# Performance work log

Measured on AMD Instinct MI355X. Metric: run time of the kernel, lower is better.

The kernel has to match this reference:

```python
import jax, jax.numpy as jnp
import numpy as np

ITERATIONS = 10
LAMBDA0 = 0.01


def skew(v):
    # (..., 3) -> (..., 3, 3) skew-symmetric matrices
    x, y, z = v[..., 0], v[..., 1], v[..., 2]
    o = jnp.zeros_like(x)
    return jnp.stack([
        jnp.stack([o, -z, y], -1),
        jnp.stack([z, o, -x], -1),
        jnp.stack([-y, x, o], -1)], -2)


def so3exp_map(w):
    # Rodrigues formula, numerically safe near theta=0
    theta2 = jnp.sum(w * w) + 1e-12
    theta = jnp.sqrt(theta2)
    W = skew(w)
    A = jnp.sin(theta) / theta
    B = (1.0 - jnp.cos(theta)) / theta2
    return jnp.eye(3, dtype=w.dtype) + A * W + B * (W @ W)


def sobel_filter(img):
    # img: (C, H, W) -> (gx, gy) each (C, H, W); depthwise conv, zero pad
    C = img.shape[0]
    kx = jnp.array([[-1., 0., 1.], [-2., 0., 2.], [-1., 0., 1.]], img.dtype)
    k = jnp.stack([kx, kx.T], 0)                       # (2,3,3)
    kern = jnp.broadcast_to(k[None, :, None], (C, 2, 1, 3, 3)).reshape(2 * C, 1, 3, 3)
    out = jax.lax.conv_general_dilated(img[None], kern, (1, 1), 'SAME',
                                       feature_group_count=C)[0]
    return out[0::2], out[1::2]


def from_homogeneous(x):
    return x[..., :-1] / x[..., -1:]


def _forward(q_matrix, r_matrix, points_2d, points_3d, query_feat, reference_feat, K1, size_ratio):
    C, H, W = query_feat.shape
    rel = q_matrix @ jnp.linalg.inv(r_matrix)
    R = rel[:3, :3]
    t = rel[3, :3]  # faithful to original (bottom row)
    gx, gy = sobel_filter(query_feat)

    idx0 = jnp.floor(points_2d / size_ratio).astype(jnp.int32)
    ix0 = jnp.clip(idx0[:, 0], 0, W - 1)
    iy0 = jnp.clip(idx0[:, 1], 0, H - 1)
    feat0 = reference_feat[:, iy0, ix0].T              # (N, C)

    pts_h = jnp.concatenate([points_3d, jnp.ones_like(points_3d[:, :1])], -1)
    pts0 = from_homogeneous(pts_h @ r_matrix.T)        # (N, 3)

    fx, fy = K1[0, 0], K1[1, 1]
    N = pts0.shape[0]
    I3 = jnp.broadcast_to(jnp.eye(3, dtype=pts0.dtype), (N, 3, 3))

    def gather_idx(p2d):
        ii = jnp.floor(p2d / size_ratio).astype(jnp.int32)
        return jnp.clip(ii[:, 0], 0, W - 1), jnp.clip(ii[:, 1], 0, H - 1)

    def step(carry, i):
        R, t, lam, prev = carry
        pts1 = pts0 @ R + t                            # (N, 3) (faithful: R, not R.T)
        ix, iy = gather_idx(from_homogeneous(pts1 @ K1.T))
        err = query_feat[:, iy, ix].T - feat0          # (N, C)
        cost = jnp.sum(err * err, -1)                  # squared_loss, weights = 1
        prev = jnp.where(i == 0, cost.mean(), prev)

        J_p_T = jnp.concatenate([I3, -skew(pts1)], -1)  # (N, 3, 6)
        x, y, z = pts1[:, 0], pts1[:, 1], pts1[:, 2]
        o, zz = jnp.ones_like(x), jnp.zeros_like(x)
        J_h_p = jnp.stack([o * fx, zz, -fx * x / z,
                           zz, o * fy, -fy * y / z], -1).reshape(N, 2, 3)
        J_h_p = J_h_p / z[:, None, None] / size_ratio   # (N, 2, 3)
        gxf = gx[:, iy, ix].T
        gyf = gy[:, iy, ix].T
        J_e_h = jnp.stack([gxf, gyf], -1)               # (N, C, 2)
        J = jnp.einsum('ncu,nuk->nck', J_e_h, J_h_p @ J_p_T)  # (N, C, 6)

        g = jnp.einsum('nck,nc->k', J, err)             # (6,)
        Hs = jnp.einsum('nck,ncl->kl', J, J)            # (6, 6)
        D = jnp.diag(jnp.diag(Hs) + 1e-9)
        delta = -(jnp.linalg.inv(Hs + D * lam) @ g)

        dt, dw = delta[:3], delta[3:6]
        dr = so3exp_map(dw)
        R_new = dr @ R
        t_new = dr @ t + dt
        npts = pts0 @ R_new.T + t_new
        jx, jy = gather_idx(from_homogeneous(npts @ K1.T))
        nerr = query_feat[:, jy, jx].T - feat0
        ncost = jnp.sum(nerr * nerr, -1).mean()

        bad = jnp.isnan(ncost) | jnp.any(jnp.isnan(delta))
        worse = ncost > prev
        lam_upd = jnp.clip(lam * jnp.where(worse, 10., 0.1), 1e-6, 100.)
        lam = jnp.where(bad, lam, lam_upd)
        accept = jnp.logical_not(worse | bad)
        R = jnp.where(accept, R_new, R)
        t = jnp.where(accept, t_new, t)
        prev = jnp.where(accept, ncost, prev)
        return (R, t, lam, prev), None

    lam0 = jnp.asarray(LAMBDA0, pts0.dtype)
    prev0 = jnp.asarray(jnp.inf, pts0.dtype)
    (R, t, _, _), _ = jax.lax.scan(step, (R, t, lam0, prev0), jnp.arange(ITERATIONS))
    return R, t


def setup_inputs() -> dict:
    key = jax.random.key(0)
    k1, k2, k3, k4, k5 = jax.random.split(key, 5)
    N, C, H, W = 8192, 1024, 128, 128
    size_ratio = 8
    f, cx, cy = 1200.0, 512.0, 512.0
    K1 = jnp.array([[f, 0., cx], [0., f, cy], [0., 0., 1.]], jnp.float32)
    # 3D points whose identity-pose projection lands inside the 1024px image
    uv = jax.random.uniform(k1, (N, 2), jnp.float32, 100.0, 900.0)
    z = jax.random.uniform(k2, (N, 1), jnp.float32, 4.0, 8.0)
    points_3d = jnp.concatenate([(uv - jnp.array([cx, cy])) / f * z, z], -1)
    points_2d = jax.random.uniform(k3, (N, 2), jnp.float32, 0.0, 1023.0)
    query_feat = jax.random.normal(k4, (C, H, W), jnp.float32) * 0.1
    reference_feat = jax.random.normal(k5, (C, H, W), jnp.float32) * 0.1
    return {
        'q_matrix': jnp.eye(4, dtype=jnp.float32),
        'r_matrix': jnp.eye(4, dtype=jnp.float32),
        'points_2d': points_2d,
        'points_3d': points_3d,
        'query_feat': query_feat,
        'reference_feat': reference_feat,
        'K1': K1,
        'size_ratio': size_ratio,
    }


def reference(q_matrix, r_matrix, points_2d, points_3d, query_feat, reference_feat, K1, size_ratio):
    return _forward(q_matrix, r_matrix, points_2d, points_3d, query_feat,
                    reference_feat, K1, size_ratio)
```

## Files before the change

kernel.cpp:

```cpp
#include <hip/hip_runtime.h>
#include <math.h>

constexpr int C_  = 1024;
constexpr int H_  = 128;
constexpr int W_  = 128;
constexpr int HW_ = H_ * W_;
constexpr int N_  = 8192;
constexpr int NCOMP = 28;
constexpr int ITERS = 10;


__global__ void k_init(const float* __restrict__ q, const float* __restrict__ r,
                       const float* __restrict__ K1, const int* __restrict__ srp,
                       float* __restrict__ st) {
    if (threadIdx.x != 0 || blockIdx.x != 0) return;
    double a[4][8];
    for (int i = 0; i < 4; i++)
        for (int j = 0; j < 4; j++) { a[i][j] = r[i*4+j]; a[i][j+4] = (i == j) ? 1.0 : 0.0; }
    for (int col = 0; col < 4; col++) {
        int piv = col; double mx = fabs(a[col][col]);
        for (int i = col+1; i < 4; i++) if (fabs(a[i][col]) > mx) { mx = fabs(a[i][col]); piv = i; }
        if (piv != col) for (int j = 0; j < 8; j++) { double t = a[col][j]; a[col][j] = a[piv][j]; a[piv][j] = t; }
        double d = a[col][col];
        for (int j = 0; j < 8; j++) a[col][j] /= d;
        for (int i = 0; i < 4; i++) if (i != col) {
            double f = a[i][col];
            for (int j = 0; j < 8; j++) a[i][j] -= f * a[col][j];
        }
    }
    double rel[4][4];
    for (int i = 0; i < 4; i++)
        for (int j = 0; j < 4; j++) {
            double s = 0;
            for (int k = 0; k < 4; k++) s += (double)q[i*4+k] * a[k][j+4];
            rel[i][j] = s;
        }
    for (int i = 0; i < 3; i++)
        for (int j = 0; j < 3; j++) st[i*3+j] = (float)rel[i][j];
    st[9]  = (float)rel[3][0];
    st[10] = (float)rel[3][1];
    st[11] = (float)rel[3][2];
    st[12] = 0.01f;
    st[13] = __builtin_inff();
    for (int i = 0; i < 9; i++) st[32+i] = K1[i];
    st[41] = K1[0]; st[42] = K1[4];
    st[43] = (float)srp[0];
}

__global__ void k_pts0(const float* __restrict__ p3d, const float* __restrict__ p2d,
                       const float* __restrict__ r, const int* __restrict__ srp,
                       float* __restrict__ pts0, int* __restrict__ pix0) {
    int n = blockIdx.x * blockDim.x + threadIdx.x;
    if (n >= N_) return;
    float sr = (float)srp[0];
    float ph[4] = { p3d[n*3+0], p3d[n*3+1], p3d[n*3+2], 1.f };
    float h[4];
    for (int i = 0; i < 4; i++) {
        float s = 0.f;
        for (int j = 0; j < 4; j++) s += r[i*4+j] * ph[j];
        h[i] = s;
    }
    pts0[n*3+0] = h[0]/h[3];
    pts0[n*3+1] = h[1]/h[3];
    pts0[n*3+2] = h[2]/h[3];
    int ix = (int)floorf(p2d[n*2+0] / sr); ix = min(max(ix, 0), W_-1);
    int iy = (int)floorf(p2d[n*2+1] / sr); iy = min(max(iy, 0), H_-1);
    pix0[n] = iy * W_ + ix;
}

template <bool SOBEL>
__global__ void k_transpose2(const float* __restrict__ src, float* __restrict__ dq,
                             float* __restrict__ dgx, float* __restrict__ dgy) {
    constexpr int CT = 16, YT = 8, XT = 32;
    constexpr int RS = YT + 2;
    constexpr int CS = XT + 2;
    constexpr int PCS = 35;
    constexpr int CHS = RS * PCS + 1;
    __shared__ float lds[CT * CHS];
    const int x0 = blockIdx.x * XT;
    const int y0 = blockIdx.y * YT;
    const int cc = blockIdx.z * CT;
    const int tid = threadIdx.x;
    for (int idx = tid; idx < CT * RS * CS; idx += 256) {
        int c   = idx / (RS * CS);
        int rem = idx % (RS * CS);
        int r   = rem / CS;
        int x   = rem % CS;
        int gy  = y0 + r - 1;
        int gx  = x0 + x - 1;
        float v = 0.f;
        if (gy >= 0 && gy < H_ && gx >= 0 && gx < W_)
            v = src[(size_t)(cc + c) * HW_ + gy * W_ + gx];
        lds[c * CHS + r * PCS + x] = v;
    }
    __syncthreads();
    const int c       = tid & 15;
    const int s       = tid >> 4;
    const int row     = s >> 1;
    const int colbase = (s & 1) * 16;
    const float* Lt = &lds[c * CHS + row * PCS + colbase];
    const float* Lm = Lt + PCS;
    const float* Lb = Lm + PCS;
    size_t o = ((size_t)((y0 + row) * W_ + x0 + colbase)) * C_ + cc + c;
    if (!SOBEL) {
        for (int cx = 0; cx < 16; cx++, o += C_)
            dq[o] = Lm[cx + 1];
    } else {
        float t0l = Lt[0], t0m = Lt[1];
        float t1l = Lm[0], t1m = Lm[1];
        float t2l = Lb[0], t2m = Lb[1];
        for (int cx = 0; cx < 16; cx++, o += C_) {
            float t0r = Lt[cx + 2];
            float t1r = Lm[cx + 2];
            float t2r = Lb[cx + 2];
            dq[o]  = t1m;
            dgx[o] = (t0r - t0l) + 2.f*(t1r - t1l) + (t2r - t2l);
            dgy[o] = (t2l + 2.f*t2m + t2r) - (t0l + 2.f*t0m + t0r);
            t0l = t0m; t0m = t0r;
            t1l = t1m; t1m = t1r;
            t2l = t2m; t2m = t2r;
        }
    }
}

__global__ void k_feat0(const float* __restrict__ rT, const int* __restrict__ pix0,
                        float* __restrict__ feat0) {
    int n = blockIdx.x;
    const float4* s = (const float4*)(rT + (size_t)pix0[n] * C_);
    float4* d = (float4*)(feat0 + (size_t)n * C_);
    d[threadIdx.x] = s[threadIdx.x];
}

__device__ inline float waveSum(float v) {
    for (int o = 32; o; o >>= 1) v += __shfl_down(v, o, 64);
    return v;
}

__global__ void k_passA(const float* __restrict__ qT, const float* __restrict__ gxT,
                        const float* __restrict__ gyT, const float* __restrict__ feat0,
                        const float* __restrict__ pts0, const float* __restrict__ st,
                        float* __restrict__ parts) {
    const int n = blockIdx.x;
    const int tid = threadIdx.x;
    const float p0 = pts0[n*3+0], p1 = pts0[n*3+1], p2 = pts0[n*3+2];
    const float X = p0*st[0] + p1*st[3] + p2*st[6] + st[9];
    const float Y = p0*st[1] + p1*st[4] + p2*st[7] + st[10];
    const float Z = p0*st[2] + p1*st[5] + p2*st[8] + st[11];
    const float hx = st[32]*X + st[33]*Y + st[34]*Z;
    const float hy = st[35]*X + st[36]*Y + st[37]*Z;
    const float hz = st[38]*X + st[39]*Y + st[40]*Z;
    const float sr = st[43];
    const float u = hx / hz, v = hy / hz;
    int ix = (int)floorf(u / sr); ix = min(max(ix, 0), W_-1);
    int iy = (int)floorf(v / sr); iy = min(max(iy, 0), H_-1);
    const int pix = iy * W_ + ix;

    const float4* q4 = (const float4*)(qT  + (size_t)pix * C_);
    const float4* g4 = (const float4*)(gxT + (size_t)pix * C_);
    const float4* h4 = (const float4*)(gyT + (size_t)pix * C_);
    const float4* f4 = (const float4*)(feat0 + (size_t)n * C_);
    float4 qv = q4[tid], gv = g4[tid], yv = h4[tid], fv = f4[tid];

    float cost = 0, bx = 0, by = 0, mxx = 0, mxy = 0, myy = 0;
    {
        float e;
        e = qv.x - fv.x; cost += e*e; bx += gv.x*e; by += yv.x*e; mxx += gv.x*gv.x; mxy += gv.x*yv.x; myy += yv.x*yv.x;
        e = qv.y - fv.y; cost += e*e; bx += gv.y*e; by += yv.y*e; mxx += gv.y*gv.y; mxy += gv.y*yv.y; myy += yv.y*yv.y;
        e = qv.z - fv.z; cost += e*e; bx += gv.z*e; by += yv.z*e; mxx += gv.z*gv.z; mxy += gv.z*yv.z; myy += yv.z*yv.z;
        e = qv.w - fv.w; cost += e*e; bx += gv.w*e; by += yv.w*e; mxx += gv.w*gv.w; mxy += gv.w*yv.w; myy += yv.w*yv.w;
    }
    cost = waveSum(cost); bx = waveSum(bx); by = waveSum(by);
    mxx = waveSum(mxx); mxy = waveSum(mxy); myy = waveSum(myy);

    __shared__ float red[4][6];
    int wid = tid >> 6, lane = tid & 63;
    if (lane == 0) {
        red[wid][0] = cost; red[wid][1] = bx;  red[wid][2] = by;
        red[wid][3] = mxx;  red[wid][4] = mxy; red[wid][5] = myy;
    }
    __syncthreads();
    if (tid == 0) {
        cost = red[0][0]+red[1][0]+red[2][0]+red[3][0];
        bx   = red[0][1]+red[1][1]+red[2][1]+red[3][1];
        by   = red[0][2]+red[1][2]+red[2][2]+red[3][2];
        mxx  = red[0][3]+red[1][3]+red[2][3]+red[3][3];
        mxy  = red[0][4]+red[1][4]+red[2][4]+red[3][4];
        myy  = red[0][5]+red[1][5]+red[2][5]+red[3][5];

        const float fx = st[41], fy = st[42];
        const float s = 1.f / (Z * sr);
        const float jh00 = fx, jh02 = -fx * X / Z;
        const float jh11 = fy, jh12 = -fy * Y / Z;
        float A0[6], A1[6];
        A0[0] = s*jh00; A0[1] = 0.f;    A0[2] = s*jh02;
        A0[3] = s*(jh02*Y); A0[4] = s*(jh00*Z - jh02*X); A0[5] = s*(-jh00*Y);
        A1[0] = 0.f;    A1[1] = s*jh11; A1[2] = s*jh12;
        A1[3] = s*(-jh11*Z + jh12*Y); A1[4] = s*(-jh12*X); A1[5] = s*(jh11*X);

        parts[0*N_ + n] = cost;
        for (int k = 0; k < 6; k++) parts[(1+k)*N_ + n] = A0[k]*bx + A1[k]*by;
        int idx = 7;
        for (int k = 0; k < 6; k++)
            for (int l = k; l < 6; l++) {
                parts[idx*N_ + n] = A0[k]*A0[l]*mxx + (A0[k]*A1[l] + A1[k]*A0[l])*mxy + A1[k]*A1[l]*myy;
                idx++;
            }
    }
}

__global__ void k_reduce_solve(const float* __restrict__ parts, float* __restrict__ st,
                               int iter) {
    const int tid = threadIdx.x;
    const int w = tid >> 6, lane = tid & 63;
    for (int comp = w; comp < NCOMP; comp += 16) {
        const float4* p4 = (const float4*)(parts + (size_t)comp * N_);
        double s = 0;
        for (int i = lane; i < N_/4; i += 64) {
            float4 v = p4[i];
            s += (double)v.x + (double)v.y + (double)v.z + (double)v.w;
        }
        for (int o = 32; o; o >>= 1) s += __shfl_down(s, o, 64);
        if (lane == 0) st[44 + comp] = (float)s;
    }
    __syncthreads();
    if (tid != 0) return;

    double costsum = st[44];
    if (iter == 0) st[13] = (float)(costsum / (double)N_);
    double g[6];
    for (int k = 0; k < 6; k++) g[k] = st[45+k];
    double Hs[6][6];
    int idx = 51;
    for (int k = 0; k < 6; k++)
        for (int l = k; l < 6; l++) { Hs[k][l] = st[idx]; Hs[l][k] = st[idx]; idx++; }
    double lam = st[12];
    double M[6][7];
    for (int i = 0; i < 6; i++) {
        for (int j = 0; j < 6; j++) M[i][j] = Hs[i][j];
        M[i][i] += (Hs[i][i] + 1e-9) * lam;
        M[i][6] = -g[i];
    }
    for (int col = 0; col < 6; col++) {
        int piv = col; double mx = fabs(M[col][col]);
        for (int i = col+1; i < 6; i++) if (fabs(M[i][col]) > mx) { mx = fabs(M[i][col]); piv = i; }
        if (piv != col) for (int j = col; j < 7; j++) { double t = M[col][j]; M[col][j] = M[piv][j]; M[piv][j] = t; }
        double d = M[col][col];
        for (int j = col; j < 7; j++) M[col][j] /= d;
        for (int i = 0; i < 6; i++) if (i != col) {
            double f = M[i][col];
            if (f != 0.0) for (int j = col; j < 7; j++) M[i][j] -= f * M[col][j];
        }
    }
    double delta[6];
    int bad = 0;
    for (int i = 0; i < 6; i++) {
        delta[i] = M[i][6];
        st[26+i] = (float)delta[i];
        if (isnan(st[26+i])) bad = 1;
    }
    st[72] = (float)bad;
    double w0 = delta[3], w1 = delta[4], w2 = delta[5];
    double th2 = w0*w0 + w1*w1 + w2*w2 + 1e-12;
    double th = sqrt(th2);
    double Af = sin(th) / th, Bf = (1.0 - cos(th)) / th2;
    double Wm[3][3] = {{0,-w2,w1},{w2,0,-w0},{-w1,w0,0}};
    double W2[3][3];
    for (int i = 0; i < 3; i++)
        for (int j = 0; j < 3; j++) {
            double s2 = 0;
            for (int k = 0; k < 3; k++) s2 += Wm[i][k]*Wm[k][j];
            W2[i][j] = s2;
        }
    double dr[3][3];
    for (int i = 0; i < 3; i++)
        for (int j = 0; j < 3; j++)
            dr[i][j] = (i == j ? 1.0 : 0.0) + Af*Wm[i][j] + Bf*W2[i][j];
    double Rn[3][3];
    for (int i = 0; i < 3; i++)
        for (int j = 0; j < 3; j++) {
            double s2 = 0;
            for (int k = 0; k < 3; k++) s2 += dr[i][k] * (double)st[k*3+j];
            Rn[i][j] = s2;
        }
    for (int i = 0; i < 3; i++)
        for (int j = 0; j < 3; j++) st[14 + i*3 + j] = (float)Rn[i][j];
    for (int i = 0; i < 3; i++) {
        double s2 = 0;
        for (int k = 0; k < 3; k++) s2 += dr[i][k] * (double)st[9+k];
        st[23+i] = (float)(s2 + delta[i]);
    }
}

__global__ void k_passB(const float* __restrict__ qT, const float* __restrict__ feat0,
                        const float* __restrict__ pts0, const float* __restrict__ st,
                        float* __restrict__ ncost) {
    const int n = blockIdx.x;
    const int tid = threadIdx.x;
    const float p0 = pts0[n*3+0], p1 = pts0[n*3+1], p2 = pts0[n*3+2];
    const float X = p0*st[14] + p1*st[15] + p2*st[16] + st[23];
    const float Y = p0*st[17] + p1*st[18] + p2*st[19] + st[24];
    const float Z = p0*st[20] + p1*st[21] + p2*st[22] + st[25];
    const float hx = st[32]*X + st[33]*Y + st[34]*Z;
    const float hy = st[35]*X + st[36]*Y + st[37]*Z;
    const float hz = st[38]*X + st[39]*Y + st[40]*Z;
    const float sr = st[43];
    const float u = hx / hz, v = hy / hz;
    int ix = (int)floorf(u / sr); ix = min(max(ix, 0), W_-1);
    int iy = (int)floorf(v / sr); iy = min(max(iy, 0), H_-1);
    const int pix = iy * W_ + ix;

    const float4* q4 = (const float4*)(qT + (size_t)pix * C_);
    const float4* f4 = (const float4*)(feat0 + (size_t)n * C_);
    float4 qv = q4[tid], fv = f4[tid];
    float cost = 0, e;
    e = qv.x - fv.x; cost += e*e;
    e = qv.y - fv.y; cost += e*e;
    e = qv.z - fv.z; cost += e*e;
    e = qv.w - fv.w; cost += e*e;
    cost = waveSum(cost);
    __shared__ float red[4];
    int wid = tid >> 6, lane = tid & 63;
    if (lane == 0) red[wid] = cost;
    __syncthreads();
    if (tid == 0) ncost[n] = red[0] + red[1] + red[2] + red[3];
}

__global__ void k_decide(const float* __restrict__ ncost, float* __restrict__ st) {
    const int tid = threadIdx.x;
    double s = 0;
    for (int i = tid; i < N_; i += 256) s += (double)ncost[i];
    __shared__ double sd[256];
    sd[tid] = s;
    __syncthreads();
    for (int k = 128; k; k >>= 1) { if (tid < k) sd[tid] += sd[tid+k]; __syncthreads(); }
    if (tid == 0) {
        float nc = (float)(sd[0] / (double)N_);
        float prev = st[13], lam = st[12];
        bool bad = isnan(nc) || (st[72] != 0.f);
        bool worse = nc > prev;
        float lu = lam * (worse ? 10.f : 0.1f);
        lu = fminf(fmaxf(lu, 1e-6f), 100.f);
        st[12] = bad ? lam : lu;
        bool accept = !(worse || bad);
        if (accept) {
            for (int i = 0; i < 9; i++) st[i] = st[14+i];
            for (int i = 0; i < 3; i++) st[9+i] = st[23+i];
            st[13] = nc;
        }
    }
}

__global__ void k_out(const float* __restrict__ st, float* __restrict__ out) {
    int i = threadIdx.x;
    if (i < 12) out[i] = st[i];
}

extern "C" void kernel_launch(void* const* d_in, const int* in_sizes, int n_in,
                              void* d_out, int out_size, void* d_ws, size_t ws_size,
                              hipStream_t stream) {
    const float* q   = (const float*)d_in[0];
    const float* r   = (const float*)d_in[1];
    const float* p2d = (const float*)d_in[2];
    const float* p3d = (const float*)d_in[3];
    const float* qf  = (const float*)d_in[4];
    const float* rf  = (const float*)d_in[5];
    const float* K1  = (const float*)d_in[6];
    const int*   srp = (const int*)d_in[7];

    float* ws = (float*)d_ws;
    size_t off = 0;
    float* qT    = ws + off; off += (size_t)HW_ * C_;
    float* gxT   = ws + off; off += (size_t)HW_ * C_;
    float* gyT   = ws + off; off += (size_t)HW_ * C_;
    float* feat0 = ws + off; off += (size_t)N_ * C_;
    float* pts0  = ws + off; off += 3 * N_;
    int*   pix0  = (int*)(ws + off); off += N_;
    float* parts = ws + off; off += (size_t)NCOMP * N_;
    float* ncost = ws + off; off += N_;
    float* st    = ws + off; off += 128;

    k_init<<<1, 1, 0, stream>>>(q, r, K1, srp, st);
    k_pts0<<<(N_ + 255) / 256, 256, 0, stream>>>(p3d, p2d, r, srp, pts0, pix0);
    k_transpose2<false><<<dim3(W_/32, H_/8, C_/16), 256, 0, stream>>>(rf, qT, nullptr, nullptr);
    k_feat0<<<N_, 256, 0, stream>>>(qT, pix0, feat0);
    k_transpose2<true><<<dim3(W_/32, H_/8, C_/16), 256, 0, stream>>>(qf, qT, gxT, gyT);

    for (int it = 0; it < ITERS; it++) {
        k_passA<<<N_, 256, 0, stream>>>(qT, gxT, gyT, feat0, pts0, st, parts);
        k_reduce_solve<<<1, 1024, 0, stream>>>(parts, st, it);
        k_passB<<<N_, 256, 0, stream>>>(qT, feat0, pts0, st, ncost);
        k_decide<<<1, 256, 0, stream>>>(ncost, st);
    }
    k_out<<<1, 64, 0, stream>>>(st, (float*)d_out);
}
```

Measured before the change: 1.049 ms.

## Map one wavefront per point, pre-reduce per block, merge setup kernels

Each 256-thread block now handles four points, one wavefront each, instead of one point per block. Wave reductions use xor shuffles, and the 28 Jacobian/Hessian components are computed in parallel across lanes and summed per block. This shrinks the partial-sum buffers that the single-block solve and decide kernels read by a factor of four. k_init and k_pts0 are merged into one launch, and the transpose tile height is halved to double the number of blocks. The cost is extra per-block shared-memory syncs, and the floating-point summation order changes.

```diff
diff --git a/kernel.cpp b/kernel.cpp
--- a/kernel.cpp
+++ b/kernel.cpp
@@ -8,70 +8,70 @@
 constexpr int N_  = 8192;
 constexpr int NCOMP = 28;
 constexpr int ITERS = 10;
-
-
-__global__ void k_init(const float* __restrict__ q, const float* __restrict__ r,
-                       const float* __restrict__ K1, const int* __restrict__ srp,
-                       float* __restrict__ st) {
-    if (threadIdx.x != 0 || blockIdx.x != 0) return;
-    double a[4][8];
-    for (int i = 0; i < 4; i++)
-        for (int j = 0; j < 4; j++) { a[i][j] = r[i*4+j]; a[i][j+4] = (i == j) ? 1.0 : 0.0; }
-    for (int col = 0; col < 4; col++) {
-        int piv = col; double mx = fabs(a[col][col]);
-        for (int i = col+1; i < 4; i++) if (fabs(a[i][col]) > mx) { mx = fabs(a[i][col]); piv = i; }
-        if (piv != col) for (int j = 0; j < 8; j++) { double t = a[col][j]; a[col][j] = a[piv][j]; a[piv][j] = t; }
-        double d = a[col][col];
-        for (int j = 0; j < 8; j++) a[col][j] /= d;
-        for (int i = 0; i < 4; i++) if (i != col) {
-            double f = a[i][col];
-            for (int j = 0; j < 8; j++) a[i][j] -= f * a[col][j];
-        }
-    }
-    double rel[4][4];
-    for (int i = 0; i < 4; i++)
-        for (int j = 0; j < 4; j++) {
-            double s = 0;
-            for (int k = 0; k < 4; k++) s += (double)q[i*4+k] * a[k][j+4];
-            rel[i][j] = s;
-        }
-    for (int i = 0; i < 3; i++)
-        for (int j = 0; j < 3; j++) st[i*3+j] = (float)rel[i][j];
-    st[9]  = (float)rel[3][0];
-    st[10] = (float)rel[3][1];
-    st[11] = (float)rel[3][2];
-    st[12] = 0.01f;
-    st[13] = __builtin_inff();
-    for (int i = 0; i < 9; i++) st[32+i] = K1[i];
-    st[41] = K1[0]; st[42] = K1[4];
-    st[43] = (float)srp[0];
-}
-
-__global__ void k_pts0(const float* __restrict__ p3d, const float* __restrict__ p2d,
-                       const float* __restrict__ r, const int* __restrict__ srp,
-                       float* __restrict__ pts0, int* __restrict__ pix0) {
+constexpr int NB_ = 2048;
+
+
+__global__ void k_setup(const float* __restrict__ q, const float* __restrict__ r,
+                        const float* __restrict__ K1, const int* __restrict__ srp,
+                        const float* __restrict__ p3d, const float* __restrict__ p2d,
+                        float* __restrict__ st, float* __restrict__ pts0,
+                        int* __restrict__ pix0) {
     int n = blockIdx.x * blockDim.x + threadIdx.x;
-    if (n >= N_) return;
-    float sr = (float)srp[0];
-    float ph[4] = { p3d[n*3+0], p3d[n*3+1], p3d[n*3+2], 1.f };
-    float h[4];
-    for (int i = 0; i < 4; i++) {
-        float s = 0.f;
-        for (int j = 0; j < 4; j++) s += r[i*4+j] * ph[j];
-        h[i] = s;
-    }
-    pts0[n*3+0] = h[0]/h[3];
-    pts0[n*3+1] = h[1]/h[3];
-    pts0[n*3+2] = h[2]/h[3];
-    int ix = (int)floorf(p2d[n*2+0] / sr); ix = min(max(ix, 0), W_-1);
-    int iy = (int)floorf(p2d[n*2+1] / sr); iy = min(max(iy, 0), H_-1);
-    pix0[n] = iy * W_ + ix;
+    if (n < N_) {
+        float sr = (float)srp[0];
+        float ph[4] = { p3d[n*3+0], p3d[n*3+1], p3d[n*3+2], 1.f };
+        float h[4];
+        for (int i = 0; i < 4; i++) {
+            float s = 0.f;
+            for (int j = 0; j < 4; j++) s += r[i*4+j] * ph[j];
+            h[i] = s;
+        }
+        pts0[n*3+0] = h[0]/h[3];
+        pts0[n*3+1] = h[1]/h[3];
+        pts0[n*3+2] = h[2]/h[3];
+        int ix = (int)floorf(p2d[n*2+0] / sr); ix = min(max(ix, 0), W_-1);
+        int iy = (int)floorf(p2d[n*2+1] / sr); iy = min(max(iy, 0), H_-1);
+        pix0[n] = iy * W_ + ix;
+    }
+    if (blockIdx.x == 0 && threadIdx.x == 0) {
+        double a[4][8];
+        for (int i = 0; i < 4; i++)
+            for (int j = 0; j < 4; j++) { a[i][j] = r[i*4+j]; a[i][j+4] = (i == j) ? 1.0 : 0.0; }
+        for (int col = 0; col < 4; col++) {
+            int piv = col; double mx = fabs(a[col][col]);
+            for (int i = col+1; i < 4; i++) if (fabs(a[i][col]) > mx) { mx = fabs(a[i][col]); piv = i; }
+            if (piv != col) for (int j = 0; j < 8; j++) { double t = a[col][j]; a[col][j] = a[piv][j]; a[piv][j] = t; }
+            double d = a[col][col];
+            for (int j = 0; j < 8; j++) a[col][j] /= d;
+            for (int i = 0; i < 4; i++) if (i != col) {
+                double f = a[i][col];
+                for (int j = 0; j < 8; j++) a[i][j] -= f * a[col][j];
+            }
+        }
+        double rel[4][4];
+        for (int i = 0; i < 4; i++)
+            for (int j = 0; j < 4; j++) {
+                double s = 0;
+                for (int k = 0; k < 4; k++) s += (double)q[i*4+k] * a[k][j+4];
+                rel[i][j] = s;
+            }
+        for (int i = 0; i < 3; i++)
+            for (int j = 0; j < 3; j++) st[i*3+j] = (float)rel[i][j];
+        st[9]  = (float)rel[3][0];
+        st[10] = (float)rel[3][1];
+        st[11] = (float)rel[3][2];
+        st[12] = 0.01f;
+        st[13] = __builtin_inff();
+        for (int i = 0; i < 9; i++) st[32+i] = K1[i];
+        st[41] = K1[0]; st[42] = K1[4];
+        st[43] = (float)srp[0];
+    }
 }
 
 template <bool SOBEL>
 __global__ void k_transpose2(const float* __restrict__ src, float* __restrict__ dq,
                              float* __restrict__ dgx, float* __restrict__ dgy) {
-    constexpr int CT = 16, YT = 8, XT = 32;
+    constexpr int CT = 16, YT = 4, XT = 32;
     constexpr int RS = YT + 2;
     constexpr int CS = XT + 2;
     constexpr int PCS = 35;
@@ -96,20 +96,20 @@
     __syncthreads();
     const int c       = tid & 15;
     const int s       = tid >> 4;
-    const int row     = s >> 1;
-    const int colbase = (s & 1) * 16;
+    const int row     = s >> 2;
+    const int colbase = (s & 3) * 8;
     const float* Lt = &lds[c * CHS + row * PCS + colbase];
     const float* Lm = Lt + PCS;
     const float* Lb = Lm + PCS;
     size_t o = ((size_t)((y0 + row) * W_ + x0 + colbase)) * C_ + cc + c;
     if (!SOBEL) {
-        for (int cx = 0; cx < 16; cx++, o += C_)
+        for (int cx = 0; cx < 8; cx++, o += C_)
             dq[o] = Lm[cx + 1];
     } else {
         float t0l = Lt[0], t0m = Lt[1];
         float t1l = Lm[0], t1m = Lm[1];
         float t2l = Lb[0], t2m = Lb[1];
-        for (int cx = 0; cx < 16; cx++, o += C_) {
+        for (int cx = 0; cx < 8; cx++, o += C_) {
             float t0r = Lt[cx + 2];
             float t1r = Lm[cx + 2];
             float t2r = Lb[cx + 2];
@@ -123,25 +123,28 @@
     }
 }
 
-__global__ void k_feat0(const float* __restrict__ rT, const int* __restrict__ pix0,
-                        float* __restrict__ feat0) {
-    int n = blockIdx.x;
+__global__ __launch_bounds__(256) void k_feat0(const float* __restrict__ rT,
+                                               const int* __restrict__ pix0,
+                                               float* __restrict__ feat0) {
+    const int w = threadIdx.x >> 6, lane = threadIdx.x & 63;
+    const int n = blockIdx.x * 4 + w;
     const float4* s = (const float4*)(rT + (size_t)pix0[n] * C_);
     float4* d = (float4*)(feat0 + (size_t)n * C_);
-    d[threadIdx.x] = s[threadIdx.x];
-}
-
-__device__ inline float waveSum(float v) {
-    for (int o = 32; o; o >>= 1) v += __shfl_down(v, o, 64);
-    return v;
-}
-
-__global__ void k_passA(const float* __restrict__ qT, const float* __restrict__ gxT,
-                        const float* __restrict__ gyT, const float* __restrict__ feat0,
-                        const float* __restrict__ pts0, const float* __restrict__ st,
-                        float* __restrict__ parts) {
-    const int n = blockIdx.x;
-    const int tid = threadIdx.x;
+#pragma unroll
+    for (int i = 0; i < 4; i++) d[i*64 + lane] = s[i*64 + lane];
+}
+
+__device__ inline float sel6(int k, float v0, float v1, float v2,
+                             float v3, float v4, float v5) {
+    return k==0 ? v0 : k==1 ? v1 : k==2 ? v2 : k==3 ? v3 : k==4 ? v4 : v5;
+}
+
+__global__ __launch_bounds__(256) void k_passA(const float* __restrict__ qT,
+        const float* __restrict__ gxT, const float* __restrict__ gyT,
+        const float* __restrict__ feat0, const float* __restrict__ pts0,
+        const float* __restrict__ st, float* __restrict__ partial) {
+    const int w = threadIdx.x >> 6, lane = threadIdx.x & 63;
+    const int n = blockIdx.x * 4 + w;
     const float p0 = pts0[n*3+0], p1 = pts0[n*3+1], p2 = pts0[n*3+2];
     const float X = p0*st[0] + p1*st[3] + p2*st[6] + st[9];
     const float Y = p0*st[1] + p1*st[4] + p2*st[7] + st[10];
@@ -159,67 +162,73 @@
     const float4* g4 = (const float4*)(gxT + (size_t)pix * C_);
     const float4* h4 = (const float4*)(gyT + (size_t)pix * C_);
     const float4* f4 = (const float4*)(feat0 + (size_t)n * C_);
-    float4 qv = q4[tid], gv = g4[tid], yv = h4[tid], fv = f4[tid];
 
     float cost = 0, bx = 0, by = 0, mxx = 0, mxy = 0, myy = 0;
-    {
+#pragma unroll
+    for (int i = 0; i < 4; i++) {
+        float4 qv = q4[i*64 + lane], gv = g4[i*64 + lane];
+        float4 yv = h4[i*64 + lane], fv = f4[i*64 + lane];
         float e;
         e = qv.x - fv.x; cost += e*e; bx += gv.x*e; by += yv.x*e; mxx += gv.x*gv.x; mxy += gv.x*yv.x; myy += yv.x*yv.x;
         e = qv.y - fv.y; cost += e*e; bx += gv.y*e; by += yv.y*e; mxx += gv.y*gv.y; mxy += gv.y*yv.y; myy += yv.y*yv.y;
         e = qv.z - fv.z; cost += e*e; bx += gv.z*e; by += yv.z*e; mxx += gv.z*gv.z; mxy += gv.z*yv.z; myy += yv.z*yv.z;
         e = qv.w - fv.w; cost += e*e; bx += gv.w*e; by += yv.w*e; mxx += gv.w*gv.w; mxy += gv.w*yv.w; myy += yv.w*yv.w;
     }
-    cost = waveSum(cost); bx = waveSum(bx); by = waveSum(by);
-    mxx = waveSum(mxx); mxy = waveSum(mxy); myy = waveSum(myy);
-
-    __shared__ float red[4][6];
-    int wid = tid >> 6, lane = tid & 63;
-    if (lane == 0) {
-        red[wid][0] = cost; red[wid][1] = bx;  red[wid][2] = by;
-        red[wid][3] = mxx;  red[wid][4] = mxy; red[wid][5] = myy;
-    }
+#pragma unroll
+    for (int off = 32; off; off >>= 1) {
+        cost += __shfl_xor(cost, off, 64);
+        bx   += __shfl_xor(bx,   off, 64);
+        by   += __shfl_xor(by,   off, 64);
+        mxx  += __shfl_xor(mxx,  off, 64);
+        mxy  += __shfl_xor(mxy,  off, 64);
+        myy  += __shfl_xor(myy,  off, 64);
+    }
+
+    const float fx = st[41], fy = st[42];
+    const float sc = 1.f / (Z * sr);
+    const float jh00 = fx, jh02 = -fx * X / Z;
+    const float jh11 = fy, jh12 = -fy * Y / Z;
+    const float a00 = sc*jh00, a01 = 0.f,     a02 = sc*jh02;
+    const float a03 = sc*(jh02*Y), a04 = sc*(jh00*Z - jh02*X), a05 = sc*(-jh00*Y);
+    const float a10 = 0.f,     a11 = sc*jh11, a12 = sc*jh12;
+    const float a13 = sc*(-jh11*Z + jh12*Y), a14 = sc*(-jh12*X), a15 = sc*(jh11*X);
+
+    float val = 0.f;
+    const int t = lane;
+    if (t == 0) {
+        val = cost;
+    } else if (t < 7) {
+        int k = t - 1;
+        val = sel6(k,a00,a01,a02,a03,a04,a05)*bx + sel6(k,a10,a11,a12,a13,a14,a15)*by;
+    } else if (t < NCOMP) {
+        int idx = t - 7, k = 0;
+        while (idx >= 6 - k) { idx -= 6 - k; k++; }
+        int l = k + idx;
+        float A0k = sel6(k,a00,a01,a02,a03,a04,a05);
+        float A1k = sel6(k,a10,a11,a12,a13,a14,a15);
+        float A0l = sel6(l,a00,a01,a02,a03,a04,a05);
+        float A1l = sel6(l,a10,a11,a12,a13,a14,a15);
+        val = A0k*A0l*mxx + (A0k*A1l + A1k*A0l)*mxy + A1k*A1l*myy;
+    }
+
+    __shared__ float pl[4][NCOMP];
+    if (t < NCOMP) pl[w][t] = val;
     __syncthreads();
-    if (tid == 0) {
-        cost = red[0][0]+red[1][0]+red[2][0]+red[3][0];
-        bx   = red[0][1]+red[1][1]+red[2][1]+red[3][1];
-        by   = red[0][2]+red[1][2]+red[2][2]+red[3][2];
-        mxx  = red[0][3]+red[1][3]+red[2][3]+red[3][3];
-        mxy  = red[0][4]+red[1][4]+red[2][4]+red[3][4];
-        myy  = red[0][5]+red[1][5]+red[2][5]+red[3][5];
-
-        const float fx = st[41], fy = st[42];
-        const float s = 1.f / (Z * sr);
-        const float jh00 = fx, jh02 = -fx * X / Z;
-        const float jh11 = fy, jh12 = -fy * Y / Z;
-        float A0[6], A1[6];
-        A0[0] = s*jh00; A0[1] = 0.f;    A0[2] = s*jh02;
-        A0[3] = s*(jh02*Y); A0[4] = s*(jh00*Z - jh02*X); A0[5] = s*(-jh00*Y);
-        A1[0] = 0.f;    A1[1] = s*jh11; A1[2] = s*jh12;
-        A1[3] = s*(-jh11*Z + jh12*Y); A1[4] = s*(-jh12*X); A1[5] = s*(jh11*X);
-
-        parts[0*N_ + n] = cost;
-        for (int k = 0; k < 6; k++) parts[(1+k)*N_ + n] = A0[k]*bx + A1[k]*by;
-        int idx = 7;
-        for (int k = 0; k < 6; k++)
-            for (int l = k; l < 6; l++) {
-                parts[idx*N_ + n] = A0[k]*A0[l]*mxx + (A0[k]*A1[l] + A1[k]*A0[l])*mxy + A1[k]*A1[l]*myy;
-                idx++;
-            }
-    }
-}
-
-__global__ void k_reduce_solve(const float* __restrict__ parts, float* __restrict__ st,
-                               int iter) {
+    if (threadIdx.x < NCOMP)
+        partial[(size_t)threadIdx.x * NB_ + blockIdx.x] =
+            pl[0][threadIdx.x] + pl[1][threadIdx.x] + pl[2][threadIdx.x] + pl[3][threadIdx.x];
+}
+
+__global__ void k_RS(const float* __restrict__ partial, float* __restrict__ st,
+                     int iter) {
     const int tid = threadIdx.x;
     const int w = tid >> 6, lane = tid & 63;
     for (int comp = w; comp < NCOMP; comp += 16) {
-        const float4* p4 = (const float4*)(parts + (size_t)comp * N_);
         double s = 0;
-        for (int i = lane; i < N_/4; i += 64) {
-            float4 v = p4[i];
-            s += (double)v.x + (double)v.y + (double)v.z + (double)v.w;
-        }
-        for (int o = 32; o; o >>= 1) s += __shfl_down(s, o, 64);
+#pragma unroll 4
+        for (int i = 0; i < NB_/64; i++)
+            s += (double)partial[(size_t)comp * NB_ + i*64 + lane];
+        for (int off = 32; off; off >>= 1) s += __shfl_down(s, off, 64);
         if (lane == 0) st[44 + comp] = (float)s;
     }
     __syncthreads();
@@ -291,11 +300,11 @@
     }
 }
 
-__global__ void k_passB(const float* __restrict__ qT, const float* __restrict__ feat0,
-                        const float* __restrict__ pts0, const float* __restrict__ st,
-                        float* __restrict__ ncost) {
-    const int n = blockIdx.x;
-    const int tid = threadIdx.x;
+__global__ __launch_bounds__(256) void k_passB(const float* __restrict__ qT,
+        const float* __restrict__ feat0, const float* __restrict__ pts0,
+        const float* __restrict__ st, float* __restrict__ ncostp) {
+    const int w = threadIdx.x >> 6, lane = threadIdx.x & 63;
+    const int n = blockIdx.x * 4 + w;
     const float p0 = pts0[n*3+0], p1 = pts0[n*3+1], p2 = pts0[n*3+2];
     const float X = p0*st[14] + p1*st[15] + p2*st[16] + st[23];
     const float Y = p0*st[17] + p1*st[18] + p2*st[19] + st[24];
@@ -311,30 +320,33 @@
 
     const float4* q4 = (const float4*)(qT + (size_t)pix * C_);
     const float4* f4 = (const float4*)(feat0 + (size_t)n * C_);
-    float4 qv = q4[tid], fv = f4[tid];
-    float cost = 0, e;
-    e = qv.x - fv.x; cost += e*e;
-    e = qv.y - fv.y; cost += e*e;
-    e = qv.z - fv.z; cost += e*e;
-    e = qv.w - fv.w; cost += e*e;
-    cost = waveSum(cost);
-    __shared__ float red[4];
-    int wid = tid >> 6, lane = tid & 63;
-    if (lane == 0) red[wid] = cost;
+    float cost = 0;
+#pragma unroll
+    for (int i = 0; i < 4; i++) {
+        float4 qv = q4[i*64 + lane], fv = f4[i*64 + lane];
+        float e;
+        e = qv.x - fv.x; cost += e*e;
+        e = qv.y - fv.y; cost += e*e;
+        e = qv.z - fv.z; cost += e*e;
+        e = qv.w - fv.w; cost += e*e;
+    }
+#pragma unroll
+    for (int off = 32; off; off >>= 1) cost += __shfl_xor(cost, off, 64);
+
+    __shared__ float pl[4];
+    if (lane == 0) pl[w] = cost;
     __syncthreads();
-    if (tid == 0) ncost[n] = red[0] + red[1] + red[2] + red[3];
-}
-
-__global__ void k_decide(const float* __restrict__ ncost, float* __restrict__ st) {
-    const int tid = threadIdx.x;
+    if (threadIdx.x == 0) ncostp[blockIdx.x] = pl[0] + pl[1] + pl[2] + pl[3];
+}
+
+__global__ void k_decide(const float* __restrict__ ncostp, float* __restrict__ st) {
+    const int lane = threadIdx.x;
     double s = 0;
-    for (int i = tid; i < N_; i += 256) s += (double)ncost[i];
-    __shared__ double sd[256];
-    sd[tid] = s;
-    __syncthreads();
-    for (int k = 128; k; k >>= 1) { if (tid < k) sd[tid] += sd[tid+k]; __syncthreads(); }
-    if (tid == 0) {
-        float nc = (float)(sd[0] / (double)N_);
+#pragma unroll 4
+    for (int i = 0; i < NB_/64; i++) s += (double)ncostp[i*64 + lane];
+    for (int off = 32; off; off >>= 1) s += __shfl_down(s, off, 64);
+    if (lane == 0) {
+        float nc = (float)(s / (double)N_);
         float prev = st[13], lam = st[12];
         bool bad = isnan(nc) || (st[72] != 0.f);
         bool worse = nc > prev;
@@ -375,21 +387,20 @@
     float* feat0 = ws + off; off += (size_t)N_ * C_;
     float* pts0  = ws + off; off += 3 * N_;
     int*   pix0  = (int*)(ws + off); off += N_;
-    float* parts = ws + off; off += (size_t)NCOMP * N_;
-    float* ncost = ws + off; off += N_;
+    float* partial = ws + off; off += (size_t)NCOMP * NB_;
+    float* ncostp  = ws + off; off += NB_;
     float* st    = ws + off; off += 128;
 
-    k_init<<<1, 1, 0, stream>>>(q, r, K1, srp, st);
-    k_pts0<<<(N_ + 255) / 256, 256, 0, stream>>>(p3d, p2d, r, srp, pts0, pix0);
-    k_transpose2<false><<<dim3(W_/32, H_/8, C_/16), 256, 0, stream>>>(rf, qT, nullptr, nullptr);
-    k_feat0<<<N_, 256, 0, stream>>>(qT, pix0, feat0);
-    k_transpose2<true><<<dim3(W_/32, H_/8, C_/16), 256, 0, stream>>>(qf, qT, gxT, gyT);
+    k_setup<<<N_/256, 256, 0, stream>>>(q, r, K1, srp, p3d, p2d, st, pts0, pix0);
+    k_transpose2<false><<<dim3(W_/32, H_/4, C_/16), 256, 0, stream>>>(rf, qT, nullptr, nullptr);
+    k_feat0<<<NB_, 256, 0, stream>>>(qT, pix0, feat0);
+    k_transpose2<true><<<dim3(W_/32, H_/4, C_/16), 256, 0, stream>>>(qf, qT, gxT, gyT);
 
     for (int it = 0; it < ITERS; it++) {
-        k_passA<<<N_, 256, 0, stream>>>(qT, gxT, gyT, feat0, pts0, st, parts);
-        k_reduce_solve<<<1, 1024, 0, stream>>>(parts, st, it);
-        k_passB<<<N_, 256, 0, stream>>>(qT, feat0, pts0, st, ncost);
-        k_decide<<<1, 256, 0, stream>>>(ncost, st);
+        k_passA<<<NB_, 256, 0, stream>>>(qT, gxT, gyT, feat0, pts0, st, partial);
+        k_RS<<<1, 1024, 0, stream>>>(partial, st, it);
+        k_passB<<<NB_, 256, 0, stream>>>(qT, feat0, pts0, st, ncostp);
+        k_decide<<<1, 64, 0, stream>>>(ncostp, st);
     }
     k_out<<<1, 64, 0, stream>>>(st, (float*)d_out);
 }
```

Result: faster. 851.8 us (-18.8%).
